# Kernel optimization log

Measured on AMD Instinct MI355X. Metric: run time of the kernel, lower is better.

## Reference

```python
import jax, jax.numpy as jnp
import numpy as np


def setup_inputs() -> dict:
    key = jax.random.key(0)
    k1, k2, k3, k4 = jax.random.split(key, 4)
    B, IN, OUT, R = 4096, 4096, 4096, 256
    x = jax.random.normal(k1, (B, IN), dtype=jnp.float32)
    U = jax.random.normal(k2, (R, IN), dtype=jnp.float32) / np.sqrt(IN)
    V = jax.random.normal(k3, (OUT, R), dtype=jnp.float32) / np.sqrt(R)
    bias = jax.random.uniform(k4, (OUT,), dtype=jnp.float32,
                              minval=-IN ** -0.5, maxval=IN ** -0.5)
    return {"x": x, "U": U, "V": V, "bias": bias}


def reference(x, U, V, bias):
    # Low-rank linear: out[b,j] = sum_k V[j,k] * (sum_i U[k,i] * x[b,i]) + bias[j]
    # (the torch loops with sparsity=1.0 / keep_stride==1 compute exactly this)
    t = jnp.einsum('bi,ri->br', x, U)        # [B, R]
    out = jnp.einsum('br,or->bo', t, V) + bias  # [B, OUT]
    return out
```

## Files before the change

### kernel.cpp

```cpp
#include <hip/hip_runtime.h>

typedef __attribute__((ext_vector_type(8))) short bf16x8;
typedef __attribute__((ext_vector_type(4))) float f32x4;

__device__ __forceinline__ unsigned short f2bf(float f) {
  unsigned int u = __float_as_uint(f);
  return (unsigned short)((u + 0x7fffu + ((u >> 16) & 1u)) >> 16);
}

__device__ __forceinline__ void gload_lds16(const void* g, void* l) {
  __builtin_amdgcn_global_load_lds((const __attribute__((address_space(1))) void*)g,
                                   (__attribute__((address_space(3))) void*)l,
                                   16, 0, 0);
}

__global__ void castUV(const float4* __restrict__ U, const float4* __restrict__ V,
                       ushort4* __restrict__ Ub, ushort4* __restrict__ Vb) {
  const int NU = 256 * 4096 / 4;
  int i = blockIdx.x * 256 + threadIdx.x;
  const float4* s; ushort4* d; int j;
  if (i < NU) { s = U; d = Ub; j = i; }
  else        { s = V; d = Vb; j = i - NU; }
  float4 v = s[j];
  ushort4 o;
  o.x = f2bf(v.x); o.y = f2bf(v.y); o.z = f2bf(v.z); o.w = f2bf(v.w);
  d[j] = o;
}

template <int MREP, int NREP, bool BIAS, bool AFP32>
__global__ __launch_bounds__(256)
void gemm_nt(const void* __restrict__ Ap,
             const unsigned short* __restrict__ B,
             const float* __restrict__ bias,
             float* __restrict__ C,
             int lda, int ldb, int ldc,
             int nkt, int kChunk, long long splitStride) {
  constexpr int BM = 32 * MREP;
  constexpr int BN = 32 * NREP;
  constexpr int ISS_A = BM / 64;
  constexpr int ISS_B = BN / 64;

  __shared__ unsigned short sA[2][BM * 32];
  __shared__ unsigned short sB[2][BN * 32];

  const int tid = threadIdx.x;
  const int l = tid & 63;
  const int w = tid >> 6;
  const int wm = (w >> 1) * (MREP * 16);
  const int wn = (w & 1) * (NREP * 16);
  const int rm = blockIdx.x * BM;
  const int rn = blockIdx.y * BN;
  const int k0base = blockIdx.z * kChunk;

  const int lr = l & 15;
  const int lc8 = (l >> 4) * 8;

  auto stage = [&](int kt, int buf) {
    const int k0 = k0base + kt * 32;
    if constexpr (AFP32) {
      const float* A32 = (const float*)Ap;
      constexpr int EPT = BM * 32 / 256;
      const int eo = tid * EPT;
      const int r = eo >> 5, c = eo & 31;
      const float* src = A32 + (long long)(rm + r) * lda + k0 + c;
      if constexpr (EPT == 4) {
        float4 v = *(const float4*)src;
        ushort4 o;
        o.x = f2bf(v.x); o.y = f2bf(v.y); o.z = f2bf(v.z); o.w = f2bf(v.w);
        *(ushort4*)&sA[buf][eo] = o;
      } else {
        float4 v0 = *(const float4*)src;
        float4 v1 = *(const float4*)(src + 4);
        ushort4 o0, o1;
        o0.x = f2bf(v0.x); o0.y = f2bf(v0.y); o0.z = f2bf(v0.z); o0.w = f2bf(v0.w);
        o1.x = f2bf(v1.x); o1.y = f2bf(v1.y); o1.z = f2bf(v1.z); o1.w = f2bf(v1.w);
        *(ushort4*)&sA[buf][eo] = o0;
        *(ushort4*)&sA[buf][eo + 4] = o1;
      }
    } else {
      const unsigned short* A = (const unsigned short*)Ap;
#pragma unroll
      for (int is = 0; is < ISS_A; ++is) {
        int eo = is * 2048 + tid * 8;
        int r = eo >> 5, c = eo & 31;
        gload_lds16(A + (long long)(rm + r) * lda + k0 + c, &sA[buf][eo]);
      }
    }
#pragma unroll
    for (int is = 0; is < ISS_B; ++is) {
      int eo = is * 2048 + tid * 8;
      int r = eo >> 5, c = eo & 31;
      gload_lds16(B + (long long)(rn + r) * ldb + k0 + c, &sB[buf][eo]);
    }
  };

  f32x4 acc[MREP][NREP] = {};

  stage(0, 0);
  for (int kt = 0; kt < nkt; ++kt) {
    __syncthreads();
    if (kt + 1 < nkt) stage(kt + 1, (kt + 1) & 1);
    const unsigned short* a0 = sA[kt & 1];
    const unsigned short* b0 = sB[kt & 1];
    bf16x8 af[MREP], bfr[NREP];
#pragma unroll
    for (int m = 0; m < MREP; ++m)
      af[m] = *(const bf16x8*)&a0[(wm + m * 16 + lr) * 32 + lc8];
#pragma unroll
    for (int n = 0; n < NREP; ++n)
      bfr[n] = *(const bf16x8*)&b0[(wn + n * 16 + lr) * 32 + lc8];
#pragma unroll
    for (int m = 0; m < MREP; ++m)
#pragma unroll
      for (int n = 0; n < NREP; ++n)
        acc[m][n] = __builtin_amdgcn_mfma_f32_16x16x32_bf16(af[m], bfr[n], acc[m][n], 0, 0, 0);
  }

  float* Cb = C + (long long)blockIdx.z * splitStride;
  const int r0 = rm + wm + (l >> 4) * 4;
  const int c0 = rn + wn + lr;
#pragma unroll
  for (int n = 0; n < NREP; ++n) {
    const int cc = c0 + n * 16;
    const float badd = BIAS ? bias[cc] : 0.0f;
#pragma unroll
    for (int m = 0; m < MREP; ++m) {
#pragma unroll
      for (int i = 0; i < 4; ++i)
        Cb[(long long)(r0 + m * 16 + i) * ldc + cc] = acc[m][n][i] + badd;
    }
  }
}

__global__ void reduce8(const float4* __restrict__ P, ushort4* __restrict__ t) {
  const int S = 4096 * 256 / 4;
  int i = blockIdx.x * 256 + threadIdx.x;
  float4 s = P[i];
#pragma unroll
  for (int z = 1; z < 8; ++z) {
    float4 v = P[i + z * S];
    s.x += v.x; s.y += v.y; s.z += v.z; s.w += v.w;
  }
  ushort4 o;
  o.x = f2bf(s.x); o.y = f2bf(s.y); o.z = f2bf(s.z); o.w = f2bf(s.w);
  t[i] = o;
}

extern "C" void kernel_launch(void* const* d_in, const int* in_sizes, int n_in,
                              void* d_out, int out_size, void* d_ws, size_t ws_size,
                              hipStream_t stream) {
  const float* x    = (const float*)d_in[0];
  const float* U    = (const float*)d_in[1];
  const float* V    = (const float*)d_in[2];
  const float* bias = (const float*)d_in[3];
  float* out = (float*)d_out;

  char* ws = (char*)d_ws;
  float* P            = (float*)ws;
  unsigned short* tb  = (unsigned short*)(ws + (32u << 20));
  unsigned short* Ub  = (unsigned short*)(ws + (34u << 20));
  unsigned short* Vb  = (unsigned short*)(ws + (36u << 20));

  castUV<<<2048, 256, 0, stream>>>((const float4*)U, (const float4*)V,
                                   (ushort4*)Ub, (ushort4*)Vb);

  dim3 g1(4096 / 32, 1, 8);
  gemm_nt<1, 8, false, true><<<g1, 256, 0, stream>>>(x, Ub, nullptr, P,
                                                     4096, 4096, 256,
                                                     16, 512,
                                                     (long long)4096 * 256);

  reduce8<<<(4096 * 256 / 4) / 256, 256, 0, stream>>>((const float4*)P, (ushort4*)tb);

  dim3 g2(4096 / 128, 4096 / 128, 1);
  gemm_nt<4, 4, true, false><<<g2, 256, 0, stream>>>(tb, Vb, bias, out,
                                                     256, 256, 4096,
                                                     8, 0, 0);
}
```

Before: 67.94 us.

## Store split-K partials in bf16, enlarge first GEMM M tile, reorder staging loads

The first GEMM now writes its eight split-K partial sums as bf16 instead of fp32, which halves the partial buffer traffic for both the GEMM epilogue and the reduction kernel. The reduction kernel converts the bf16 partials back to fp32 before summing them. The first GEMM's M tile goes from 32 to 64 rows, halving the grid and cutting repeated loads of the U tile. B-tile async loads are also issued before the fp32 A-tile conversion. Rounding the partials to bf16 adds some error to the low-rank intermediate.

After: 60.84 us. 1.12x faster.

```diff
diff --git a/kernel.cpp b/kernel.cpp
--- a/kernel.cpp
+++ b/kernel.cpp
@@ -6,6 +6,10 @@
 __device__ __forceinline__ unsigned short f2bf(float f) {
   unsigned int u = __float_as_uint(f);
   return (unsigned short)((u + 0x7fffu + ((u >> 16) & 1u)) >> 16);
+}
+
+__device__ __forceinline__ float bf2f(unsigned short s) {
+  return __uint_as_float(((unsigned int)s) << 16);
 }
 
 __device__ __forceinline__ void gload_lds16(const void* g, void* l) {
@@ -27,12 +31,12 @@
   d[j] = o;
 }
 
-template <int MREP, int NREP, bool BIAS, bool AFP32>
+template <int MREP, int NREP, bool BIAS, bool AFP32, bool OUT_BF16>
 __global__ __launch_bounds__(256)
 void gemm_nt(const void* __restrict__ Ap,
              const unsigned short* __restrict__ B,
              const float* __restrict__ bias,
-             float* __restrict__ C,
+             void* __restrict__ Cv,
              int lda, int ldb, int ldc,
              int nkt, int kChunk, long long splitStride) {
   constexpr int BM = 32 * MREP;
@@ -57,6 +61,12 @@
 
   auto stage = [&](int kt, int buf) {
     const int k0 = k0base + kt * 32;
+#pragma unroll
+    for (int is = 0; is < ISS_B; ++is) {
+      int eo = is * 2048 + tid * 8;
+      int r = eo >> 5, c = eo & 31;
+      gload_lds16(B + (long long)(rn + r) * ldb + k0 + c, &sB[buf][eo]);
+    }
     if constexpr (AFP32) {
       const float* A32 = (const float*)Ap;
       constexpr int EPT = BM * 32 / 256;
@@ -86,12 +96,6 @@
         gload_lds16(A + (long long)(rm + r) * lda + k0 + c, &sA[buf][eo]);
       }
     }
-#pragma unroll
-    for (int is = 0; is < ISS_B; ++is) {
-      int eo = is * 2048 + tid * 8;
-      int r = eo >> 5, c = eo & 31;
-      gload_lds16(B + (long long)(rn + r) * ldb + k0 + c, &sB[buf][eo]);
-    }
   };
 
   f32x4 acc[MREP][NREP] = {};
@@ -116,33 +120,45 @@
         acc[m][n] = __builtin_amdgcn_mfma_f32_16x16x32_bf16(af[m], bfr[n], acc[m][n], 0, 0, 0);
   }
 
-  float* Cb = C + (long long)blockIdx.z * splitStride;
   const int r0 = rm + wm + (l >> 4) * 4;
   const int c0 = rn + wn + lr;
+  if constexpr (OUT_BF16) {
+    unsigned short* Cb = (unsigned short*)Cv + (long long)blockIdx.z * splitStride;
 #pragma unroll
-  for (int n = 0; n < NREP; ++n) {
-    const int cc = c0 + n * 16;
-    const float badd = BIAS ? bias[cc] : 0.0f;
+    for (int n = 0; n < NREP; ++n) {
+      const int cc = c0 + n * 16;
 #pragma unroll
-    for (int m = 0; m < MREP; ++m) {
+      for (int m = 0; m < MREP; ++m)
 #pragma unroll
-      for (int i = 0; i < 4; ++i)
-        Cb[(long long)(r0 + m * 16 + i) * ldc + cc] = acc[m][n][i] + badd;
+        for (int i = 0; i < 4; ++i)
+          Cb[(long long)(r0 + m * 16 + i) * ldc + cc] = f2bf(acc[m][n][i]);
+    }
+  } else {
+    float* Cb = (float*)Cv + (long long)blockIdx.z * splitStride;
+#pragma unroll
+    for (int n = 0; n < NREP; ++n) {
+      const int cc = c0 + n * 16;
+      const float badd = BIAS ? bias[cc] : 0.0f;
+#pragma unroll
+      for (int m = 0; m < MREP; ++m)
+#pragma unroll
+        for (int i = 0; i < 4; ++i)
+          Cb[(long long)(r0 + m * 16 + i) * ldc + cc] = acc[m][n][i] + badd;
     }
   }
 }
 
-__global__ void reduce8(const float4* __restrict__ P, ushort4* __restrict__ t) {
+__global__ void reduce8(const ushort4* __restrict__ P, ushort4* __restrict__ t) {
   const int S = 4096 * 256 / 4;
   int i = blockIdx.x * 256 + threadIdx.x;
-  float4 s = P[i];
+  float sx = 0, sy = 0, sz = 0, sw = 0;
 #pragma unroll
-  for (int z = 1; z < 8; ++z) {
-    float4 v = P[i + z * S];
-    s.x += v.x; s.y += v.y; s.z += v.z; s.w += v.w;
+  for (int z = 0; z < 8; ++z) {
+    ushort4 v = P[i + z * S];
+    sx += bf2f(v.x); sy += bf2f(v.y); sz += bf2f(v.z); sw += bf2f(v.w);
   }
   ushort4 o;
-  o.x = f2bf(s.x); o.y = f2bf(s.y); o.z = f2bf(s.z); o.w = f2bf(s.w);
+  o.x = f2bf(sx); o.y = f2bf(sy); o.z = f2bf(sz); o.w = f2bf(sw);
   t[i] = o;
 }
 
@@ -156,24 +172,23 @@
   float* out = (float*)d_out;
 
   char* ws = (char*)d_ws;
-  float* P            = (float*)ws;
-  unsigned short* tb  = (unsigned short*)(ws + (32u << 20));
-  unsigned short* Ub  = (unsigned short*)(ws + (34u << 20));
-  unsigned short* Vb  = (unsigned short*)(ws + (36u << 20));
+  unsigned short* P   = (unsigned short*)ws;
+  unsigned short* tb  = (unsigned short*)(ws + (16u << 20));
+  unsigned short* Ub  = (unsigned short*)(ws + (18u << 20));
+  unsigned short* Vb  = (unsigned short*)(ws + (20u << 20));
 
   castUV<<<2048, 256, 0, stream>>>((const float4*)U, (const float4*)V,
                                    (ushort4*)Ub, (ushort4*)Vb);
 
-  dim3 g1(4096 / 32, 1, 8);
-  gemm_nt<1, 8, false, true><<<g1, 256, 0, stream>>>(x, Ub, nullptr, P,
-                                                     4096, 4096, 256,
-                                                     16, 512,
-                                                     (long long)4096 * 256);
+  dim3 g1(4096 / 64, 1, 8);
+  gemm_nt<2, 8, false, true, true><<<g1, 256, 0, stream>>>(
+      x, Ub, nullptr, P, 4096, 4096, 256,
+      16, 512, (long long)4096 * 256);
 
-  reduce8<<<(4096 * 256 / 4) / 256, 256, 0, stream>>>((const float4*)P, (ushort4*)tb);
+  reduce8<<<(4096 * 256 / 4) / 256, 256, 0, stream>>>((const ushort4*)P, (ushort4*)tb);
 
   dim3 g2(4096 / 128, 4096 / 128, 1);
-  gemm_nt<4, 4, true, false><<<g2, 256, 0, stream>>>(tb, Vb, bias, out,
-                                                     256, 256, 4096,
-                                                     8, 0, 0);
+  gemm_nt<4, 4, true, false, false><<<g2, 256, 0, stream>>>(
+      tb, Vb, bias, out, 256, 256, 4096,
+      8, 0, 0);
 }
```
